# Kernel tuning notes

Hardware: AMD Instinct MI355X
Metric: run time of the kernel (lower is better)

## Reference

```python
import jax, jax.numpy as jnp
import numpy as np

EPS = 1e-12

def l2norm(x, axis):
    # torch.nn.functional.normalize: x / max(||x||_2, eps)
    n = jnp.sqrt(jnp.sum(x * x, axis=axis, keepdims=True))
    return x / jnp.maximum(n, EPS)

def setup_inputs() -> dict:
    key = jax.random.key(0)
    k1, k2, k3, k4 = jax.random.split(key, 4)
    B, Cf, H, W = 128, 1024, 16, 16
    n_att, dv = 312, 300
    img = jax.random.normal(k1, (B, Cf, H, W), dtype=jnp.float32)
    # V is initialized from row-normalized w2v embeddings in the module
    V = l2norm(jax.random.normal(k2, (n_att, dv), dtype=jnp.float32), axis=1)
    W1 = jax.random.normal(k3, (dv, Cf), dtype=jnp.float32)
    W2 = jax.random.normal(k4, (dv, Cf), dtype=jnp.float32)
    return {"img": img, "V": V, "W1": W1, "W2": W2}

def reference(img, V, W1, W2):
    vv = l2norm(V, axis=1)                               # [i, v]
    B, Cf, H, Wd = img.shape
    av = l2norm(img.reshape(B, Cf, H * Wd), axis=1)      # [b, f, r]
    Q = vv @ W1                                          # [i, f]
    A = jnp.einsum('if,bfr->bir', Q, av)                 # attention logits
    A = jax.nn.softmax(A, axis=-1)
    F_p = jnp.einsum('bir,bfr->bif', A, av)              # attended features
    Pred_att = jnp.einsum('if,bif->bi', vv @ W2, F_p)
    return Pred_att
```

## Files before the change

### kernel.cpp

```cpp
#include <hip/hip_runtime.h>
#include <math.h>

#define NB   128
#define CF   1024
#define RR   256
#define NA   312
#define DV   300
#define M2   320
#define MT   640
#define NKC  32

typedef _Float16 half8  __attribute__((ext_vector_type(8)));
typedef float float16v  __attribute__((ext_vector_type(16)));

__global__ void k_prep(const float* __restrict__ img, float* __restrict__ invg,
                       _Float16* __restrict__ avT) {
    int rc = blockIdx.x, b = blockIdx.y;
    int r0 = rc * 64;
    int t = threadIdx.x;
    __shared__ __align__(16) char sm[64 * 65 * 4];
    _Float16 (*tile)[65] = (_Float16 (*)[65])sm;
    float    (*ssb)[65]  = (float    (*)[65])sm;
    int fl = t >> 2, cg = t & 3;
    int rl = t >> 2, g  = t & 3;
    float ss[16];
    #pragma unroll
    for (int j = 0; j < 16; ++j) ss[j] = 0.f;

    for (int cc = 0; cc < 16; ++cc) {
        int f0 = cc * 64;
        const float4* p4 = (const float4*)(img + ((size_t)(b * CF + f0 + fl)) * RR + r0 + cg * 16);
        float4 v0 = p4[0], v1 = p4[1], v2 = p4[2], v3 = p4[3];
        __syncthreads();
        float xs[16] = {v0.x, v0.y, v0.z, v0.w, v1.x, v1.y, v1.z, v1.w,
                        v2.x, v2.y, v2.z, v2.w, v3.x, v3.y, v3.z, v3.w};
        #pragma unroll
        for (int j = 0; j < 16; ++j) {
            ss[j] += xs[j] * xs[j];
            tile[fl][cg * 16 + j] = (_Float16)xs[j];
        }
        __syncthreads();
        int kc  = (f0 >> 5) + (g >> 1);
        int kkb = (g & 1) * 16;
        half8 o0, o1;
        #pragma unroll
        for (int j = 0; j < 8; ++j) o0[j] = tile[g * 16 + j][rl];
        #pragma unroll
        for (int j = 0; j < 8; ++j) o1[j] = tile[g * 16 + 8 + j][rl];
        _Float16* q = avT + (((size_t)(b * NKC + kc) * RR + r0 + rl) * 32 + kkb);
        *(half8*)q       = o0;
        *(half8*)(q + 8) = o1;
    }
    __syncthreads();
    #pragma unroll
    for (int j = 0; j < 16; ++j) ssb[fl][cg * 16 + j] = ss[j];
    __syncthreads();
    if (t < 64) {
        float tot = 0.f;
        for (int f2 = 0; f2 < 64; ++f2) tot += ssb[f2][t];
        invg[b * RR + r0 + t] = 1.f / fmaxf(sqrtf(tot), 1e-12f);
    }
}

__global__ void k_q(const float* __restrict__ V, const float* __restrict__ W1,
                    const float* __restrict__ W2, _Float16* __restrict__ Qb) {
    int ib = blockIdx.x;
    int f  = blockIdx.y * 256 + threadIdx.x;
    int t  = threadIdx.x;
    bool isQ2 = ib >= 80;
    int i0l = (ib - (isQ2 ? 80 : 0)) * 4;
    int i0g = (isQ2 ? M2 : 0) + i0l;
    __shared__ float inv4[4];
    float acc[4] = {0, 0, 0, 0};
    bool zero = (i0l >= NA);
    if (!zero) {
        int row = t >> 6, l64 = t & 63;
        float s = 0.f;
        for (int v = l64; v < DV; v += 64) { float x = V[(i0l + row) * DV + v]; s += x * x; }
        #pragma unroll
        for (int o = 32; o; o >>= 1) s += __shfl_xor(s, o, 64);
        if (l64 == 0) inv4[row] = 1.f / fmaxf(sqrtf(s), 1e-12f);
        __syncthreads();
        const float* W = isQ2 ? W2 : W1;
        for (int v = 0; v < DV; v += 4) {
            float w0 = W[(size_t)(v + 0) * CF + f];
            float w1 = W[(size_t)(v + 1) * CF + f];
            float w2 = W[(size_t)(v + 2) * CF + f];
            float w3 = W[(size_t)(v + 3) * CF + f];
            #pragma unroll
            for (int ii = 0; ii < 4; ++ii) {
                const float* Vr = V + (size_t)(i0l + ii) * DV + v;
                acc[ii] += Vr[0] * w0 + Vr[1] * w1 + Vr[2] * w2 + Vr[3] * w3;
            }
        }
        #pragma unroll
        for (int ii = 0; ii < 4; ++ii) acc[ii] *= inv4[ii];
    }
    #pragma unroll
    for (int ii = 0; ii < 4; ++ii)
        Qb[((size_t)(f >> 5) * MT + (i0g + ii)) * 32 + (f & 31)] = (_Float16)acc[ii];
}

__launch_bounds__(256, 2)
__global__ void k_gemm(const _Float16* __restrict__ Qb, const _Float16* __restrict__ avT,
                       const float* __restrict__ invg, float* __restrict__ out) {
    int lin  = blockIdx.x;
    int xcd  = lin & 7;
    int slot = lin >> 3;
    int bq   = slot / 5;
    int t2   = slot - bq * 5;
    int b    = bq * 8 + xcd;

    int tid = threadIdx.x;
    int lane = tid & 63, w = tid >> 6;
    int nl = lane & 31, kh = lane >> 5;

    __shared__ __align__(16) char smem[49152];
    _Float16* A0 = (_Float16*)smem;
    _Float16* A1 = (_Float16*)(smem + 8192);
    _Float16* B0 = (_Float16*)(smem + 16384);
    _Float16* B1 = (_Float16*)(smem + 32768);
    float* mred = (float*)smem;
    float* mg   = (float*)(smem + 1024);
    float* sred = (float*)(smem + 1280);
    float* dred = (float*)(smem + 2304);

    float16v acc[4][2];
    #pragma unroll
    for (int i = 0; i < 4; ++i)
        #pragma unroll
        for (int j = 0; j < 2; ++j)
            #pragma unroll
            for (int gi = 0; gi < 16; ++gi) acc[i][j][gi] = 0.f;

    int arow  = tid & 127;
    int akb0  = tid >> 7;
    int grow  = (arow < 64) ? (t2 * 64 + arow) : (M2 + t2 * 64 + (arow - 64));
    size_t a_src0 = (size_t)grow * 32 + akb0 * 8;
    size_t a_dst0 = ((size_t)akb0 * 128 + arow) * 8;
    size_t b_src0 = (size_t)tid * 32;
    size_t b_dst0 = (size_t)tid * 8;
    const _Float16* bpanel = avT + (size_t)b * NKC * RR * 32;

    half8 aR0[2], bR0[4], aR1[2], bR1[4];

    #define STAGE_LOAD(kc_, Av, Bv) do {                                        \
        int kcl = ((kc_) < NKC) ? (kc_) : (NKC - 1);                            \
        const _Float16* as = Qb + (size_t)kcl * MT * 32;                        \
        (Av)[0] = *(const half8*)(as + a_src0);                                 \
        (Av)[1] = *(const half8*)(as + a_src0 + 16);                            \
        const _Float16* bs = bpanel + (size_t)kcl * RR * 32;                    \
        (Bv)[0] = *(const half8*)(bs + b_src0 + 0 * 8);                         \
        (Bv)[1] = *(const half8*)(bs + b_src0 + 1 * 8);                         \
        (Bv)[2] = *(const half8*)(bs + b_src0 + 2 * 8);                         \
        (Bv)[3] = *(const half8*)(bs + b_src0 + 3 * 8);                         \
    } while (0)

    #define STAGE_WRITE(Av, Bv, Ad, Bd) do {                                    \
        *(half8*)((Ad) + a_dst0)        = (Av)[0];                              \
        *(half8*)((Ad) + a_dst0 + 2048) = (Av)[1];                              \
        *(half8*)((Bd) + b_dst0 + 0 * 2048) = (Bv)[0];                          \
        *(half8*)((Bd) + b_dst0 + 1 * 2048) = (Bv)[1];                          \
        *(half8*)((Bd) + b_dst0 + 2 * 2048) = (Bv)[2];                          \
        *(half8*)((Bd) + b_dst0 + 3 * 2048) = (Bv)[3];                          \
    } while (0)

    #define COMPUTE(Al, Bl) do {                                                \
        _Pragma("unroll")                                                       \
        for (int ks = 0; ks < 2; ++ks) {                                        \
            int kb = ks * 2 + kh;                                               \
            half8 b0f = *(const half8*)((Bl) + ((size_t)kb * 256 + w * 64 + nl) * 8);       \
            half8 b1f = *(const half8*)((Bl) + ((size_t)kb * 256 + w * 64 + 32 + nl) * 8);  \
            _Pragma("unroll")                                                   \
            for (int rf = 0; rf < 4; ++rf) {                                    \
                half8 af = *(const half8*)((Al) + ((size_t)kb * 128 + rf * 32 + nl) * 8);   \
                acc[rf][0] = __builtin_amdgcn_mfma_f32_32x32x16_f16(af, b0f, acc[rf][0], 0, 0, 0); \
                acc[rf][1] = __builtin_amdgcn_mfma_f32_32x32x16_f16(af, b1f, acc[rf][1], 0, 0, 0); \
            }                                                                   \
        }                                                                       \
    } while (0)

    STAGE_LOAD(0, aR0, bR0);
    STAGE_LOAD(1, aR1, bR1);
    STAGE_WRITE(aR0, bR0, A0, B0);

    for (int kc = 0; kc < NKC; kc += 2) {
        __syncthreads();
        STAGE_WRITE(aR1, bR1, A1, B1);
        STAGE_LOAD(kc + 2, aR0, bR0);
        COMPUTE(A0, B0);
        __syncthreads();
        if (kc + 2 < NKC) STAGE_WRITE(aR0, bR0, A0, B0);
        STAGE_LOAD(kc + 3, aR1, bR1);
        COMPUTE(A1, B1);
    }
    __syncthreads();
    #undef STAGE_LOAD
    #undef STAGE_WRITE
    #undef COMPUTE

    float iv0 = invg[b * RR + w * 64 + nl];
    float iv1 = invg[b * RR + w * 64 + 32 + nl];
    #pragma unroll
    for (int rf = 0; rf < 4; ++rf)
        #pragma unroll
        for (int gi = 0; gi < 16; ++gi) {
            acc[rf][0][gi] *= iv0;
            acc[rf][1][gi] *= iv1;
        }

    float mx[2][16];
    #pragma unroll
    for (int p = 0; p < 2; ++p)
        #pragma unroll
        for (int gi = 0; gi < 16; ++gi)
            mx[p][gi] = fmaxf(acc[p][0][gi], acc[p][1][gi]);
    #pragma unroll
    for (int off = 1; off <= 16; off <<= 1)
        #pragma unroll
        for (int p = 0; p < 2; ++p)
            #pragma unroll
            for (int gi = 0; gi < 16; ++gi)
                mx[p][gi] = fmaxf(mx[p][gi], __shfl_xor(mx[p][gi], off, 64));
    if (nl == 0) {
        #pragma unroll
        for (int p = 0; p < 2; ++p)
            #pragma unroll
            for (int gi = 0; gi < 16; ++gi) {
                int row = (gi & 3) + 8 * (gi >> 2) + 4 * kh;
                mred[(p * 32 + row) * 4 + w] = mx[p][gi];
            }
    }
    __syncthreads();
    if (tid < 64)
        mg[tid] = fmaxf(fmaxf(mred[tid * 4], mred[tid * 4 + 1]),
                        fmaxf(mred[tid * 4 + 2], mred[tid * 4 + 3]));
    __syncthreads();
    float sp[2][16], dp[2][16];
    #pragma unroll
    for (int p = 0; p < 2; ++p)
        #pragma unroll
        for (int gi = 0; gi < 16; ++gi) {
            int row = (gi & 3) + 8 * (gi >> 2) + 4 * kh;
            float m  = mg[p * 32 + row];
            float e0 = __expf(acc[p][0][gi] - m);
            float e1 = __expf(acc[p][1][gi] - m);
            sp[p][gi] = e0 + e1;
            dp[p][gi] = e0 * acc[p + 2][0][gi] + e1 * acc[p + 2][1][gi];
        }
    #pragma unroll
    for (int off = 1; off <= 16; off <<= 1)
        #pragma unroll
        for (int p = 0; p < 2; ++p)
            #pragma unroll
            for (int gi = 0; gi < 16; ++gi) {
                sp[p][gi] += __shfl_xor(sp[p][gi], off, 64);
                dp[p][gi] += __shfl_xor(dp[p][gi], off, 64);
            }
    if (nl == 0) {
        #pragma unroll
        for (int p = 0; p < 2; ++p)
            #pragma unroll
            for (int gi = 0; gi < 16; ++gi) {
                int row = (gi & 3) + 8 * (gi >> 2) + 4 * kh;
                sred[(p * 32 + row) * 4 + w] = sp[p][gi];
                dred[(p * 32 + row) * 4 + w] = dp[p][gi];
            }
    }
    __syncthreads();
    if (tid < 64) {
        float s = sred[tid * 4] + sred[tid * 4 + 1] + sred[tid * 4 + 2] + sred[tid * 4 + 3];
        float d = dred[tid * 4] + dred[tid * 4 + 1] + dred[tid * 4 + 2] + dred[tid * 4 + 3];
        int ig = t2 * 64 + tid;
        if (ig < NA) out[b * NA + ig] = d / s;
    }
}

extern "C" void kernel_launch(void* const* d_in, const int* in_sizes, int n_in,
                              void* d_out, int out_size, void* d_ws, size_t ws_size,
                              hipStream_t stream) {
    const float* img = (const float*)d_in[0];
    const float* V   = (const float*)d_in[1];
    const float* W1  = (const float*)d_in[2];
    const float* W2  = (const float*)d_in[3];
    float* out = (float*)d_out;

    char* ws = (char*)d_ws;
    size_t off = 0;
    float*    invg = (float*)(ws + off);    off += (size_t)NB * RR * 4;
    _Float16* avT  = (_Float16*)(ws + off); off += (size_t)NB * CF * RR * 2;
    _Float16* Qb   = (_Float16*)(ws + off); off += (size_t)NKC * MT * 32 * 2;

    k_prep<<<dim3(4, NB), 256, 0, stream>>>(img, invg, avT);
    k_q<<<dim3(160, 4), 256, 0, stream>>>(V, W1, W2, Qb);
    k_gemm<<<dim3(640), 256, 0, stream>>>(Qb, avT, invg, out);
}
```

Before: 301.8 us.

## Merge prep and Q kernels, use direct global-to-LDS loads in GEMM

```diff
diff --git a/kernel.cpp b/kernel.cpp
--- a/kernel.cpp
+++ b/kernel.cpp
@@ -12,98 +12,97 @@
 
 typedef _Float16 half8  __attribute__((ext_vector_type(8)));
 typedef float float16v  __attribute__((ext_vector_type(16)));
-
-__global__ void k_prep(const float* __restrict__ img, float* __restrict__ invg,
-                       _Float16* __restrict__ avT) {
-    int rc = blockIdx.x, b = blockIdx.y;
-    int r0 = rc * 64;
-    int t = threadIdx.x;
-    __shared__ __align__(16) char sm[64 * 65 * 4];
-    _Float16 (*tile)[65] = (_Float16 (*)[65])sm;
-    float    (*ssb)[65]  = (float    (*)[65])sm;
-    int fl = t >> 2, cg = t & 3;
-    int rl = t >> 2, g  = t & 3;
-    float ss[16];
-    #pragma unroll
-    for (int j = 0; j < 16; ++j) ss[j] = 0.f;
-
-    for (int cc = 0; cc < 16; ++cc) {
-        int f0 = cc * 64;
-        const float4* p4 = (const float4*)(img + ((size_t)(b * CF + f0 + fl)) * RR + r0 + cg * 16);
-        float4 v0 = p4[0], v1 = p4[1], v2 = p4[2], v3 = p4[3];
-        __syncthreads();
-        float xs[16] = {v0.x, v0.y, v0.z, v0.w, v1.x, v1.y, v1.z, v1.w,
-                        v2.x, v2.y, v2.z, v2.w, v3.x, v3.y, v3.z, v3.w};
-        #pragma unroll
-        for (int j = 0; j < 16; ++j) {
-            ss[j] += xs[j] * xs[j];
-            tile[fl][cg * 16 + j] = (_Float16)xs[j];
-        }
-        __syncthreads();
-        int kc  = (f0 >> 5) + (g >> 1);
-        int kkb = (g & 1) * 16;
-        half8 o0, o1;
-        #pragma unroll
-        for (int j = 0; j < 8; ++j) o0[j] = tile[g * 16 + j][rl];
-        #pragma unroll
-        for (int j = 0; j < 8; ++j) o1[j] = tile[g * 16 + 8 + j][rl];
-        _Float16* q = avT + (((size_t)(b * NKC + kc) * RR + r0 + rl) * 32 + kkb);
-        *(half8*)q       = o0;
-        *(half8*)(q + 8) = o1;
-    }
-    __syncthreads();
-    #pragma unroll
-    for (int j = 0; j < 16; ++j) ssb[fl][cg * 16 + j] = ss[j];
-    __syncthreads();
-    if (t < 64) {
-        float tot = 0.f;
-        for (int f2 = 0; f2 < 64; ++f2) tot += ssb[f2][t];
-        invg[b * RR + r0 + t] = 1.f / fmaxf(sqrtf(tot), 1e-12f);
-    }
-}
-
-__global__ void k_q(const float* __restrict__ V, const float* __restrict__ W1,
-                    const float* __restrict__ W2, _Float16* __restrict__ Qb) {
-    int ib = blockIdx.x;
-    int f  = blockIdx.y * 256 + threadIdx.x;
-    int t  = threadIdx.x;
-    bool isQ2 = ib >= 80;
-    int i0l = (ib - (isQ2 ? 80 : 0)) * 4;
-    int i0g = (isQ2 ? M2 : 0) + i0l;
-    __shared__ float inv4[4];
-    float acc[4] = {0, 0, 0, 0};
-    bool zero = (i0l >= NA);
-    if (!zero) {
-        int row = t >> 6, l64 = t & 63;
-        float s = 0.f;
-        for (int v = l64; v < DV; v += 64) { float x = V[(i0l + row) * DV + v]; s += x * x; }
-        #pragma unroll
-        for (int o = 32; o; o >>= 1) s += __shfl_xor(s, o, 64);
-        if (l64 == 0) inv4[row] = 1.f / fmaxf(sqrtf(s), 1e-12f);
-        __syncthreads();
-        const float* W = isQ2 ? W2 : W1;
-        for (int v = 0; v < DV; v += 4) {
-            float w0 = W[(size_t)(v + 0) * CF + f];
-            float w1 = W[(size_t)(v + 1) * CF + f];
-            float w2 = W[(size_t)(v + 2) * CF + f];
-            float w3 = W[(size_t)(v + 3) * CF + f];
-            #pragma unroll
-            for (int ii = 0; ii < 4; ++ii) {
-                const float* Vr = V + (size_t)(i0l + ii) * DV + v;
-                acc[ii] += Vr[0] * w0 + Vr[1] * w1 + Vr[2] * w2 + Vr[3] * w3;
-            }
-        }
-        #pragma unroll
-        for (int ii = 0; ii < 4; ++ii) acc[ii] *= inv4[ii];
-    }
-    #pragma unroll
-    for (int ii = 0; ii < 4; ++ii)
-        Qb[((size_t)(f >> 5) * MT + (i0g + ii)) * 32 + (f & 31)] = (_Float16)acc[ii];
+typedef float float4v   __attribute__((ext_vector_type(4)));
+
+__device__ __forceinline__ void gll16(const void* g, void* l) {
+    __builtin_amdgcn_global_load_lds(
+        (const __attribute__((address_space(1))) void*)g,
+        (__attribute__((address_space(3))) void*)l, 16, 0, 0);
+}
+
+__global__ void k_pq(const float* __restrict__ img, float* __restrict__ ssq4,
+                     _Float16* __restrict__ avT,
+                     const float* __restrict__ V, const float* __restrict__ W1,
+                     const float* __restrict__ W2, _Float16* __restrict__ Qb) {
+    int lin = blockIdx.x;
+    if (lin < 512) {
+        int q = lin & 3, b = lin >> 2;
+        int t = threadIdx.x;
+        int kk8 = t & 3;
+        int rq  = t >> 2;
+        float ss0 = 0.f, ss1 = 0.f, ss2 = 0.f, ss3 = 0.f;
+        int kc0 = q * 8;
+        for (int kc = kc0; kc < kc0 + 8; ++kc) {
+            const float* src = img + ((size_t)b * CF + kc * 32 + kk8 * 8) * RR + rq * 4;
+            float4v v[8];
+            #pragma unroll
+            for (int j = 0; j < 8; ++j) v[j] = *(const float4v*)(src + (size_t)j * RR);
+            #pragma unroll
+            for (int j = 0; j < 8; ++j) {
+                ss0 += v[j][0] * v[j][0]; ss1 += v[j][1] * v[j][1];
+                ss2 += v[j][2] * v[j][2]; ss3 += v[j][3] * v[j][3];
+            }
+            _Float16* dst = avT + ((size_t)(b * NKC + kc) * RR + rq * 4) * 32 + kk8 * 8;
+            #pragma unroll
+            for (int s = 0; s < 4; ++s) {
+                half8 o;
+                #pragma unroll
+                for (int j = 0; j < 8; ++j) o[j] = (_Float16)v[j][s];
+                *(half8*)(dst + (size_t)s * 32) = o;
+            }
+        }
+        ss0 += __shfl_xor(ss0, 1, 64); ss0 += __shfl_xor(ss0, 2, 64);
+        ss1 += __shfl_xor(ss1, 1, 64); ss1 += __shfl_xor(ss1, 2, 64);
+        ss2 += __shfl_xor(ss2, 1, 64); ss2 += __shfl_xor(ss2, 2, 64);
+        ss3 += __shfl_xor(ss3, 1, 64); ss3 += __shfl_xor(ss3, 2, 64);
+        if (kk8 == 0) {
+            float4v sv; sv[0] = ss0; sv[1] = ss1; sv[2] = ss2; sv[3] = ss3;
+            *(float4v*)(ssq4 + ((size_t)b * 4 + q) * RR + rq * 4) = sv;
+        }
+    } else {
+        int m   = lin - 512;
+        int ib  = m % 160;
+        int fch = m / 160;
+        int t   = threadIdx.x;
+        int f   = fch * 256 + t;
+        bool isQ2 = ib >= 80;
+        int i0l = (ib - (isQ2 ? 80 : 0)) * 4;
+        int i0g = (isQ2 ? M2 : 0) + i0l;
+        __shared__ float inv4[4];
+        float acc[4] = {0, 0, 0, 0};
+        bool zero = (i0l >= NA);
+        if (!zero) {
+            int row = t >> 6, l64 = t & 63;
+            float s = 0.f;
+            for (int v = l64; v < DV; v += 64) { float x = V[(i0l + row) * DV + v]; s += x * x; }
+            #pragma unroll
+            for (int o = 32; o; o >>= 1) s += __shfl_xor(s, o, 64);
+            if (l64 == 0) inv4[row] = 1.f / fmaxf(sqrtf(s), 1e-12f);
+            __syncthreads();
+            const float* W = isQ2 ? W2 : W1;
+            for (int v = 0; v < DV; v += 4) {
+                float w0 = W[(size_t)(v + 0) * CF + f];
+                float w1 = W[(size_t)(v + 1) * CF + f];
+                float w2 = W[(size_t)(v + 2) * CF + f];
+                float w3 = W[(size_t)(v + 3) * CF + f];
+                #pragma unroll
+                for (int ii = 0; ii < 4; ++ii) {
+                    const float* Vr = V + (size_t)(i0l + ii) * DV + v;
+                    acc[ii] += Vr[0] * w0 + Vr[1] * w1 + Vr[2] * w2 + Vr[3] * w3;
+                }
+            }
+            #pragma unroll
+            for (int ii = 0; ii < 4; ++ii) acc[ii] *= inv4[ii];
+        }
+        #pragma unroll
+        for (int ii = 0; ii < 4; ++ii)
+            Qb[((size_t)(f >> 5) * MT + (i0g + ii)) * 32 + (f & 31)] = (_Float16)acc[ii];
+    }
 }
 
 __launch_bounds__(256, 2)
 __global__ void k_gemm(const _Float16* __restrict__ Qb, const _Float16* __restrict__ avT,
-                       const float* __restrict__ invg, float* __restrict__ out) {
+                       const float* __restrict__ ssq4, float* __restrict__ out) {
     int lin  = blockIdx.x;
     int xcd  = lin & 7;
     int slot = lin >> 3;
@@ -137,70 +136,72 @@
     int akb0  = tid >> 7;
     int grow  = (arow < 64) ? (t2 * 64 + arow) : (M2 + t2 * 64 + (arow - 64));
     size_t a_src0 = (size_t)grow * 32 + akb0 * 8;
-    size_t a_dst0 = ((size_t)akb0 * 128 + arow) * 8;
-    size_t b_src0 = (size_t)tid * 32;
-    size_t b_dst0 = (size_t)tid * 8;
     const _Float16* bpanel = avT + (size_t)b * NKC * RR * 32;
 
-    half8 aR0[2], bR0[4], aR1[2], bR1[4];
-
-    #define STAGE_LOAD(kc_, Av, Bv) do {                                        \
-        int kcl = ((kc_) < NKC) ? (kc_) : (NKC - 1);                            \
-        const _Float16* as = Qb + (size_t)kcl * MT * 32;                        \
-        (Av)[0] = *(const half8*)(as + a_src0);                                 \
-        (Av)[1] = *(const half8*)(as + a_src0 + 16);                            \
-        const _Float16* bs = bpanel + (size_t)kcl * RR * 32;                    \
-        (Bv)[0] = *(const half8*)(bs + b_src0 + 0 * 8);                         \
-        (Bv)[1] = *(const half8*)(bs + b_src0 + 1 * 8);                         \
-        (Bv)[2] = *(const half8*)(bs + b_src0 + 2 * 8);                         \
-        (Bv)[3] = *(const half8*)(bs + b_src0 + 3 * 8);                         \
+    #define STAGE(kc_, Ab, Bb) do {                                                  \
+        const _Float16* as_ = Qb + (size_t)(kc_) * MT * 32 + a_src0;                 \
+        gll16(as_,      (char*)(Ab) + tid * 16);                                     \
+        gll16(as_ + 16, (char*)(Ab) + tid * 16 + 4096);                              \
+        const _Float16* bs_ = bpanel + (size_t)(kc_) * RR * 32 + (size_t)tid * 32;   \
+        gll16(bs_,      (char*)(Bb) + tid * 16);                                     \
+        gll16(bs_ + 8,  (char*)(Bb) + tid * 16 + 4096);                              \
+        gll16(bs_ + 16, (char*)(Bb) + tid * 16 + 8192);                              \
+        gll16(bs_ + 24, (char*)(Bb) + tid * 16 + 12288);                             \
     } while (0)
 
-    #define STAGE_WRITE(Av, Bv, Ad, Bd) do {                                    \
-        *(half8*)((Ad) + a_dst0)        = (Av)[0];                              \
-        *(half8*)((Ad) + a_dst0 + 2048) = (Av)[1];                              \
-        *(half8*)((Bd) + b_dst0 + 0 * 2048) = (Bv)[0];                          \
-        *(half8*)((Bd) + b_dst0 + 1 * 2048) = (Bv)[1];                          \
-        *(half8*)((Bd) + b_dst0 + 2 * 2048) = (Bv)[2];                          \
-        *(half8*)((Bd) + b_dst0 + 3 * 2048) = (Bv)[3];                          \
-    } while (0)
-
-    #define COMPUTE(Al, Bl) do {                                                \
-        _Pragma("unroll")                                                       \
-        for (int ks = 0; ks < 2; ++ks) {                                        \
-            int kb = ks * 2 + kh;                                               \
+    #define COMPUTE(Al, Bl) do {                                                     \
+        _Pragma("unroll")                                                            \
+        for (int ks = 0; ks < 2; ++ks) {                                             \
+            int kb = ks * 2 + kh;                                                    \
             half8 b0f = *(const half8*)((Bl) + ((size_t)kb * 256 + w * 64 + nl) * 8);       \
             half8 b1f = *(const half8*)((Bl) + ((size_t)kb * 256 + w * 64 + 32 + nl) * 8);  \
-            _Pragma("unroll")                                                   \
-            for (int rf = 0; rf < 4; ++rf) {                                    \
+            _Pragma("unroll")                                                        \
+            for (int rf = 0; rf < 4; ++rf) {                                         \
                 half8 af = *(const half8*)((Al) + ((size_t)kb * 128 + rf * 32 + nl) * 8);   \
                 acc[rf][0] = __builtin_amdgcn_mfma_f32_32x32x16_f16(af, b0f, acc[rf][0], 0, 0, 0); \
                 acc[rf][1] = __builtin_amdgcn_mfma_f32_32x32x16_f16(af, b1f, acc[rf][1], 0, 0, 0); \
-            }                                                                   \
-        }                                                                       \
+            }                                                                        \
+        }                                                                            \
     } while (0)
 
-    STAGE_LOAD(0, aR0, bR0);
-    STAGE_LOAD(1, aR1, bR1);
-    STAGE_WRITE(aR0, bR0, A0, B0);
-
-    for (int kc = 0; kc < NKC; kc += 2) {
-        __syncthreads();
-        STAGE_WRITE(aR1, bR1, A1, B1);
-        STAGE_LOAD(kc + 2, aR0, bR0);
+    STAGE(0, A0, B0);
+    STAGE(1, A1, B1);
+    asm volatile("s_waitcnt vmcnt(6)" ::: "memory");
+    __builtin_amdgcn_s_barrier();
+    __builtin_amdgcn_sched_barrier(0);
+
+    #pragma unroll 1
+    for (int kc = 0; kc < NKC - 2; kc += 2) {
         COMPUTE(A0, B0);
-        __syncthreads();
-        if (kc + 2 < NKC) STAGE_WRITE(aR0, bR0, A0, B0);
-        STAGE_LOAD(kc + 3, aR1, bR1);
+        __builtin_amdgcn_s_barrier();
+        __builtin_amdgcn_sched_barrier(0);
+        STAGE(kc + 2, A0, B0);
+        asm volatile("s_waitcnt vmcnt(6)" ::: "memory");
+        __builtin_amdgcn_s_barrier();
+        __builtin_amdgcn_sched_barrier(0);
         COMPUTE(A1, B1);
-    }
-    __syncthreads();
-    #undef STAGE_LOAD
-    #undef STAGE_WRITE
+        __builtin_amdgcn_s_barrier();
+        __builtin_amdgcn_sched_barrier(0);
+        STAGE(kc + 3, A1, B1);
+        asm volatile("s_waitcnt vmcnt(6)" ::: "memory");
+        __builtin_amdgcn_s_barrier();
+        __builtin_amdgcn_sched_barrier(0);
+    }
+    COMPUTE(A0, B0);
+    asm volatile("s_waitcnt vmcnt(0)" ::: "memory");
+    __builtin_amdgcn_s_barrier();
+    __builtin_amdgcn_sched_barrier(0);
+    COMPUTE(A1, B1);
+
+    #undef STAGE
     #undef COMPUTE
 
-    float iv0 = invg[b * RR + w * 64 + nl];
-    float iv1 = invg[b * RR + w * 64 + 32 + nl];
+    const float* sq = ssq4 + (size_t)b * 4 * RR;
+    int c0 = w * 64 + nl;
+    float p0 = sq[c0]      + sq[RR + c0]      + sq[2 * RR + c0]      + sq[3 * RR + c0];
+    float p1 = sq[32 + c0] + sq[RR + 32 + c0] + sq[2 * RR + 32 + c0] + sq[3 * RR + 32 + c0];
+    float iv0 = 1.f / fmaxf(sqrtf(p0), 1e-12f);
+    float iv1 = 1.f / fmaxf(sqrtf(p1), 1e-12f);
     #pragma unroll
     for (int rf = 0; rf < 4; ++rf)
         #pragma unroll
@@ -287,11 +288,10 @@
 
     char* ws = (char*)d_ws;
     size_t off = 0;
-    float*    invg = (float*)(ws + off);    off += (size_t)NB * RR * 4;
+    float*    ssq4 = (float*)(ws + off);    off += (size_t)NB * 4 * RR * 4;
     _Float16* avT  = (_Float16*)(ws + off); off += (size_t)NB * CF * RR * 2;
     _Float16* Qb   = (_Float16*)(ws + off); off += (size_t)NKC * MT * 32 * 2;
 
-    k_prep<<<dim3(4, NB), 256, 0, stream>>>(img, invg, avT);
-    k_q<<<dim3(160, 4), 256, 0, stream>>>(V, W1, W2, Qb);
-    k_gemm<<<dim3(640), 256, 0, stream>>>(Qb, avT, invg, out);
-}
+    k_pq<<<dim3(1152), 256, 0, stream>>>(img, ssq4, avT, V, W1, W2, Qb);
+    k_gemm<<<dim3(640), 256, 0, stream>>>(Qb, avT, ssq4, out);
+}
```

After: 277.7 us. 8.0% less time.
